# Performance work log

Hardware: AMD Instinct MI355X
Metric: run time of the kernel (lower is better)

Reference implementation:

```python
import jax, jax.numpy as jnp
import numpy as np

# Dims / scalars (from init_kwargs: m = int(T/dt), delta = dt, theta_star = threshold)
M = 50000
N = 500
DELTA = 0.001
GLEAK = 1.0
TAUS = 10.0
THETA_STAR = 1.0
SPIKE_PROB = 0.02  # sparse binary spike raster as produced by time2spike


def setup_inputs() -> dict:
    key = jax.random.key(0)
    k1, k2, k3 = jax.random.split(key, 3)
    # binary spike raster [m, n]
    spikes = (jax.random.uniform(k1, (M, N)) < SPIKE_PROB).astype(jnp.float32)
    # synapse weights ~ N(w_mean=0.01, 0.01)
    w = (0.01 + 0.01 * jax.random.normal(k2, (N,))).astype(jnp.float32)
    # reversal potentials: half excitatory (ex=5), half inhibitory (inh=-1), shuffled
    vrev = jnp.where(jax.random.uniform(k3, (N,)) < 0.5, 5.0, -1.0).astype(jnp.float32)
    return {"spikes": spikes, "w": w, "vrev": vrev}


def reference(spikes, w, vrev):
    dtype = spikes.dtype
    decay = jnp.exp(jnp.asarray(-1.0 / TAUS, dtype))

    # _compute_exp: exp_temp[i] = (exp_temp[i-1] + spikes[i-1]) * exp(-1/taus), exp_temp[0] = 0
    def exp_step(carry, s):
        nxt = (carry + s) * decay
        return nxt, nxt

    _, e_tail = jax.lax.scan(exp_step, jnp.zeros((N,), dtype), spikes[:-1])
    exp_temp = jnp.concatenate([jnp.zeros((1, N), dtype), e_tail], axis=0)  # [M, N]

    # Gsyn_pre = |w| * exp_temp ; Isyn_pre = Vrev * |w| * exp_temp.
    # Only their per-timestep sums over synapses enter the vtr recurrence,
    # so contract over n immediately instead of materializing [M, N] products.
    absw = jnp.abs(w)
    g_sum = exp_temp @ absw            # [M] = sum_j Gsyn_pre[i, j]
    i_sum = exp_temp @ (vrev * absw)   # [M] = sum_j Isyn_pre[i, j]
    a = DELTA * (GLEAK + g_sum)        # per-step leak+conductance factor
    b = DELTA * i_sum                  # per-step input drive

    # _computevtr: if vtr[i-1] < theta: vtr[i] = vtr[i-1]*(1 - a[i-1]) + b[i-1]
    # else vtr[i] stays 0 (state reset after threshold crossing), vtr[0] = 0.
    def vtr_step(v, ab):
        ai, bi = ab
        nxt = jnp.where(v < THETA_STAR, v * (1.0 - ai) + bi, jnp.asarray(0.0, dtype))
        return nxt, nxt

    _, v_tail = jax.lax.scan(vtr_step, jnp.asarray(0.0, dtype), (a[:-1], b[:-1]))
    vtr = jnp.concatenate([jnp.zeros((1,), dtype), v_tail])  # [M]
    return vtr
```

## Files before the change

kernel.cpp:

```cpp
#include <hip/hip_runtime.h>
#include <cmath>

namespace {
constexpr int NELEM  = 50000;
constexpr int NSYN   = 500;
constexpr int NQ4    = 125;
constexpr int T      = 1024;
constexpr int SBLK   = 49;
constexpr int SLOTS  = SBLK * T;
constexpr int CMAXC  = (NELEM - 1) >> 6;
constexpr int NCH_PAD = 784;
constexpr int MAXSEG = 4096;
constexpr int NGRP   = NELEM / 8;
constexpr double DELTA_D = 1.0e-3;
constexpr double THETA_D = 1.0;
constexpr float  DECAY_F = 0.90483741803595957311f;
}

struct WS {
    double2 pq[SLOTS];
    double  eAm[SLOTS], eAg[SLOTS], eAi[SLOTS];
    double  ePl[SLOTS], eQl[SLOTS];
    double  rarr[SLOTS];
    double  gAm[64], gAg[64], gAi[64];
    double  gEm[64], gEg[64], gEi[64];
    double  gPp[64], gPq[64];
    double  gEp[64], gEq[64];
    double  gmaxR[1024];
    double  gbndQ[MAXSEG];
    int     gbnd[MAXSEG];
    int     gnseg;
    int     pad;
    float   swv[SLOTS];
    float   iwv[SLOTS];
};

__global__ __launch_bounds__(256) void k_rowdot(
    const float* __restrict__ spikes,
    const float* __restrict__ w,
    const float* __restrict__ vrev,
    float* __restrict__ swv,
    float* __restrict__ iwv)
{
    const int lane = threadIdx.x & 63;
    const int wv   = threadIdx.x >> 6;
    const int rg   = blockIdx.x * 4 + wv;
    if (rg >= NGRP) return;
    const int row0 = rg * 8;

    const float4* __restrict__ w4 = reinterpret_cast<const float4*>(w);
    const float4* __restrict__ r4 = reinterpret_cast<const float4*>(vrev);
    const int j1 = lane;
    const int j2 = lane + 64;
    const bool has2 = (j2 < NQ4);
    float4 a1 = w4[j1], r1 = r4[j1];
    float4 aw1 = make_float4(fabsf(a1.x), fabsf(a1.y), fabsf(a1.z), fabsf(a1.w));
    float4 ar1 = make_float4(aw1.x * r1.x, aw1.y * r1.y, aw1.z * r1.z, aw1.w * r1.w);
    float4 aw2 = make_float4(0.f, 0.f, 0.f, 0.f), ar2 = aw2;
    if (has2) {
        float4 a2 = w4[j2], r2 = r4[j2];
        aw2 = make_float4(fabsf(a2.x), fabsf(a2.y), fabsf(a2.z), fabsf(a2.w));
        ar2 = make_float4(aw2.x * r2.x, aw2.y * r2.y, aw2.z * r2.z, aw2.w * r2.w);
    }

    float sp[8], ip[8];
#pragma unroll
    for (int r = 0; r < 8; ++r) {
        const float4* __restrict__ srow =
            reinterpret_cast<const float4*>(spikes + (size_t)(row0 + r) * NSYN);
        float4 s1 = srow[j1];
        float a = s1.x * aw1.x + s1.y * aw1.y + s1.z * aw1.z + s1.w * aw1.w;
        float b = s1.x * ar1.x + s1.y * ar1.y + s1.z * ar1.z + s1.w * ar1.w;
        if (has2) {
            float4 s2 = srow[j2];
            a += s2.x * aw2.x + s2.y * aw2.y + s2.z * aw2.z + s2.w * aw2.w;
            b += s2.x * ar2.x + s2.y * ar2.y + s2.z * ar2.z + s2.w * ar2.w;
        }
        sp[r] = a; ip[r] = b;
    }
#pragma unroll
    for (int d = 32; d > 0; d >>= 1) {
#pragma unroll
        for (int r = 0; r < 8; ++r) {
            sp[r] += __shfl_xor(sp[r], d);
            ip[r] += __shfl_xor(ip[r], d);
        }
    }
    if (lane == 0) {
        *reinterpret_cast<float4*>(swv + row0)     = make_float4(sp[0], sp[1], sp[2], sp[3]);
        *reinterpret_cast<float4*>(swv + row0 + 4) = make_float4(sp[4], sp[5], sp[6], sp[7]);
        *reinterpret_cast<float4*>(iwv + row0)     = make_float4(ip[0], ip[1], ip[2], ip[3]);
        *reinterpret_cast<float4*>(iwv + row0 + 4) = make_float4(ip[4], ip[5], ip[6], ip[7]);
    }
}

__global__ __launch_bounds__(1024) void k_scanA(const float* __restrict__ swv,
                                                const float* __restrict__ iwv,
                                                WS* __restrict__ ws)
{
    const int tid = threadIdx.x, lane = tid & 63, wv = tid >> 6, blk = blockIdx.x;
    const int idx = blk * T + tid;
    const bool live = (idx < NELEM);
    const double decay = (double)DECAY_F;
    __shared__ double s_a[16], s_b[16], s_c[16];

    double s = live ? (double)swv[idx] : 0.0;
    double t = live ? (double)iwv[idx] : 0.0;
    double m_in = live ? decay : 1.0;
    double g_in = live ? s * decay : 0.0;
    double i_in = live ? t * decay : 0.0;
#pragma unroll
    for (int d = 1; d < 64; d <<= 1) {
        double pm = __shfl_up(m_in, d);
        double pg = __shfl_up(g_in, d);
        double pi = __shfl_up(i_in, d);
        if (lane >= d) {
            g_in = m_in * pg + g_in;
            i_in = m_in * pi + i_in;
            m_in = pm * m_in;
        }
    }
    if (lane == 63) { s_a[wv] = m_in; s_b[wv] = g_in; s_c[wv] = i_in; }
    __syncthreads();
    if (wv == 0) {
        double wm = (lane < 16) ? s_a[lane] : 1.0;
        double wg = (lane < 16) ? s_b[lane] : 0.0;
        double wi = (lane < 16) ? s_c[lane] : 0.0;
#pragma unroll
        for (int d = 1; d < 16; d <<= 1) {
            double pm = __shfl_up(wm, d);
            double pg = __shfl_up(wg, d);
            double pi = __shfl_up(wi, d);
            if (lane >= d) {
                wg = wm * pg + wg;
                wi = wm * pi + wi;
                wm = pm * wm;
            }
        }
        if (lane < 16) { s_a[lane] = wm; s_b[lane] = wg; s_c[lane] = wi; }
        if (lane == 15) { ws->gAm[blk] = wm; ws->gAg[blk] = wg; ws->gAi[blk] = wi; }
    }
    __syncthreads();
    double em = __shfl_up(m_in, 1), eg = __shfl_up(g_in, 1), ei = __shfl_up(i_in, 1);
    if (lane == 0) { em = 1.0; eg = 0.0; ei = 0.0; }
    if (wv > 0) {
        double qm = s_a[wv - 1], qg = s_b[wv - 1], qi = s_c[wv - 1];
        eg = em * qg + eg;
        ei = em * qi + ei;
        em = qm * em;
    }
    ws->eAm[idx] = em; ws->eAg[idx] = eg; ws->eAi[idx] = ei;
}

__global__ void k_aggA(WS* __restrict__ ws)
{
    const int lane = threadIdx.x;
    double am = (lane < SBLK) ? ws->gAm[lane] : 1.0;
    double ag = (lane < SBLK) ? ws->gAg[lane] : 0.0;
    double ai = (lane < SBLK) ? ws->gAi[lane] : 0.0;
#pragma unroll
    for (int d = 1; d < 64; d <<= 1) {
        double pm = __shfl_up(am, d);
        double pg = __shfl_up(ag, d);
        double pi = __shfl_up(ai, d);
        if (lane >= d) {
            ag = am * pg + ag;
            ai = am * pi + ai;
            am = pm * am;
        }
    }
    double em = __shfl_up(am, 1), eg = __shfl_up(ag, 1), ei = __shfl_up(ai, 1);
    if (lane == 0) { em = 1.0; eg = 0.0; ei = 0.0; }
    if (lane < SBLK) { ws->gEm[lane] = em; ws->gEg[lane] = eg; ws->gEi[lane] = ei; }
}

__global__ __launch_bounds__(1024) void k_scanB(WS* __restrict__ ws)
{
    const int tid = threadIdx.x, lane = tid & 63, wv = tid >> 6, blk = blockIdx.x;
    const int idx = blk * T + tid;
    const bool live = (idx < NELEM);
    __shared__ double s_a[16], s_b[16];

    double em = ws->eAm[idx], eg = ws->eAg[idx], ei = ws->eAi[idx];
    double qm = ws->gEm[blk], qg = ws->gEg[blk], qi = ws->gEi[blk];
    double Eg = em * qg + eg;
    double Ei = em * qi + ei;
    (void)qm;

    double p_in = 1.0, q_in = 0.0;
    if (live) {
        double aa = DELTA_D * (1.0 + Eg);
        double om = 1.0 - aa;
        p_in = om;
        q_in = (DELTA_D * Ei) / om;
    }
#pragma unroll
    for (int d = 1; d < 64; d <<= 1) {
        double pp = __shfl_up(p_in, d);
        double pq = __shfl_up(q_in, d);
        if (lane >= d) {
            q_in = pq + q_in / pp;
            p_in = pp * p_in;
        }
    }
    if (lane == 63) { s_a[wv] = p_in; s_b[wv] = q_in; }
    __syncthreads();
    if (wv == 0) {
        double wp = (lane < 16) ? s_a[lane] : 1.0;
        double wq = (lane < 16) ? s_b[lane] : 0.0;
#pragma unroll
        for (int d = 1; d < 16; d <<= 1) {
            double pp = __shfl_up(wp, d);
            double pq = __shfl_up(wq, d);
            if (lane >= d) {
                wq = pq + wq / pp;
                wp = pp * wp;
            }
        }
        if (lane < 16) { s_a[lane] = wp; s_b[lane] = wq; }
        if (lane == 15) { ws->gPp[blk] = wp; ws->gPq[blk] = wq; }
    }
    __syncthreads();
    double ep = __shfl_up(p_in, 1), eq = __shfl_up(q_in, 1);
    if (lane == 0) { ep = 1.0; eq = 0.0; }
    if (wv > 0) {
        double ap = s_a[wv - 1], aq = s_b[wv - 1];
        eq = aq + eq / ap;
        ep = ap * ep;
    }
    ws->ePl[idx] = ep; ws->eQl[idx] = eq;
}

__global__ void k_aggB(WS* __restrict__ ws)
{
    const int lane = threadIdx.x;
    double ap = (lane < SBLK) ? ws->gPp[lane] : 1.0;
    double aq = (lane < SBLK) ? ws->gPq[lane] : 0.0;
#pragma unroll
    for (int d = 1; d < 64; d <<= 1) {
        double pp = __shfl_up(ap, d);
        double pq = __shfl_up(aq, d);
        if (lane >= d) {
            aq = pq + aq / pp;
            ap = pp * ap;
        }
    }
    double ep = __shfl_up(ap, 1), eq = __shfl_up(aq, 1);
    if (lane == 0) { ep = 1.0; eq = 0.0; }
    if (lane < SBLK) { ws->gEp[lane] = ep; ws->gEq[lane] = eq; }
}

__global__ __launch_bounds__(1024) void k_apply(WS* __restrict__ ws)
{
    const int tid = threadIdx.x, lane = tid & 63, blk = blockIdx.x;
    const int idx = blk * T + tid;
    const bool live = (idx < NELEM);

    double pl = ws->ePl[idx], ql = ws->eQl[idx];
    double ap = ws->gEp[blk], aq = ws->gEq[blk];
    double Q = aq + ql / ap;
    double P = ap * pl;
    ws->pq[idx] = make_double2(P, Q);
    double R = live ? (Q - THETA_D / P) : -1.0e308;
    ws->rarr[idx] = R;
    double mR = R;
#pragma unroll
    for (int d = 32; d > 0; d >>= 1) mR = fmax(mR, __shfl_xor(mR, d));
    if (lane == 0) ws->gmaxR[idx >> 6] = mR;
}

__global__ __launch_bounds__(1024) void k_search(WS* __restrict__ ws)
{
    const int tid = threadIdx.x;
    __shared__ double smax[NCH_PAD];
    __shared__ double s_guard;

    for (int c = tid; c < NCH_PAD; c += T)
        smax[c] = (c <= CMAXC) ? ws->gmaxR[c] : -1.0e308;
    double acc = 0.0;
    for (int i = tid; i < NELEM; i += T) acc += ws->rarr[i];
    for (int i = tid; i < NELEM; i += T) acc += ws->pq[i].y;
    if (acc == -1.2345e300) s_guard = acc;
    __syncthreads();

    if (tid < 64) {
        const int lane = tid;
        int nseg = 1;
        if (lane == 0) { ws->gbnd[0] = 0; ws->gbndQ[0] = 0.0; }
        double Qr = 0.0;
        int pos = 1;
        while (pos < NELEM && nseg < MAXSEG) {
            int c = pos >> 6;
            int i0 = -1;
            while (true) {
                int cf = -1;
                for (int cb = c; cb <= CMAXC; cb += 64) {
                    int cc = cb + lane;
                    bool qy = (cc <= CMAXC) && (smax[cc] >= Qr);
                    unsigned long long m = __ballot(qy);
                    if (m) { cf = cb + __builtin_ctzll(m); break; }
                }
                if (cf < 0) break;
                int i = (cf << 6) + lane;
                bool valid = (i >= pos) && (i < NELEM);
                double rv = valid ? ws->rarr[i] : -1.0e308;
                unsigned long long m2 = __ballot(valid && (rv >= Qr));
                if (m2) { i0 = (cf << 6) + __builtin_ctzll(m2); break; }
                c = cf + 1;
                if (c > CMAXC) break;
            }
            if (i0 < 0) break;
            int nb = i0 + 1;
            if (nb >= NELEM) break;
            Qr = ws->pq[nb].y;
            if (lane == 0) { ws->gbnd[nseg] = nb; ws->gbndQ[nseg] = Qr; }
            nseg++;
            pos = nb + 1;
        }
        if (lane == 0) ws->gnseg = nseg;
    }
}

__global__ __launch_bounds__(1024) void k_fill(const WS* __restrict__ ws,
                                               float* __restrict__ out)
{
    __shared__ int    sb[MAXSEG];
    __shared__ double sq[MAXSEG];
    __shared__ int    s_nseg;
    const int tid = threadIdx.x;
    if (tid == 0) s_nseg = ws->gnseg;
    __syncthreads();
    const int nseg = s_nseg;
    for (int i = tid; i < nseg; i += T) { sb[i] = ws->gbnd[i]; sq[i] = ws->gbndQ[i]; }
    __syncthreads();

    const int idx = blockIdx.x * T + tid;
    if (idx < NELEM) {
        int lo = 0, hi = nseg - 1;
        while (lo < hi) {
            int mid = (lo + hi + 1) >> 1;
            if (sb[mid] <= idx) lo = mid; else hi = mid - 1;
        }
        if (idx == sb[lo]) {
            out[idx] = 0.0f;
        } else {
            double2 pl = ws->pq[idx];
            out[idx] = (float)(pl.x * (pl.y - sq[lo]));
        }
    }
}

extern "C" void kernel_launch(void* const* d_in, const int* in_sizes, int n_in,
                              void* d_out, int out_size, void* d_ws, size_t ws_size,
                              hipStream_t stream) {
    const float* spikes = (const float*)d_in[0];
    const float* w      = (const float*)d_in[1];
    const float* vrev   = (const float*)d_in[2];
    float* out = (float*)d_out;
    WS* ws = (WS*)d_ws;

    hipLaunchKernelGGL(k_rowdot, dim3((NGRP + 3) / 4), dim3(256), 0, stream,
                       spikes, w, vrev, ws->swv, ws->iwv);
    hipLaunchKernelGGL(k_scanA,  dim3(SBLK), dim3(T),  0, stream, ws->swv, ws->iwv, ws);
    hipLaunchKernelGGL(k_aggA,   dim3(1),    dim3(64), 0, stream, ws);
    hipLaunchKernelGGL(k_scanB,  dim3(SBLK), dim3(T),  0, stream, ws);
    hipLaunchKernelGGL(k_aggB,   dim3(1),    dim3(64), 0, stream, ws);
    hipLaunchKernelGGL(k_apply,  dim3(SBLK), dim3(T),  0, stream, ws);
    hipLaunchKernelGGL(k_search, dim3(1),    dim3(T),  0, stream, ws);
    hipLaunchKernelGGL(k_fill,   dim3(SBLK), dim3(T),  0, stream, ws, out);
}
```

Measured before the change: 206.3 us.

## Fuse scan, aggregate and apply stages into one cooperative kernel with grid syncs

Merges the five kernels k_scanA, k_aggA, k_scanB, k_aggB and k_apply into one cooperative kernel that uses grid.sync between phases. Each block rescans the 49 block aggregates itself instead of reading results from a separate kernel. This removes four kernel launches and the intermediate global arrays (eAm/eAg/eAi, ePl/eQl). It also writes Q to a separate contiguous qarr so the search kernel reads it with better access. The cost is two grid-wide barriers, and correctness depends on all 49 blocks being co-resident.

```diff
diff --git a/kernel.cpp b/kernel.cpp
--- a/kernel.cpp
+++ b/kernel.cpp
@@ -1,5 +1,8 @@
 #include <hip/hip_runtime.h>
+#include <hip/hip_cooperative_groups.h>
 #include <cmath>
+
+namespace cg = cooperative_groups;
 
 namespace {
 constexpr int NELEM  = 50000;
@@ -19,13 +22,10 @@
 
 struct WS {
     double2 pq[SLOTS];
-    double  eAm[SLOTS], eAg[SLOTS], eAi[SLOTS];
-    double  ePl[SLOTS], eQl[SLOTS];
     double  rarr[SLOTS];
+    double  qarr[SLOTS];
     double  gAm[64], gAg[64], gAi[64];
-    double  gEm[64], gEg[64], gEi[64];
     double  gPp[64], gPq[64];
-    double  gEp[64], gEq[64];
     double  gmaxR[1024];
     double  gbndQ[MAXSEG];
     int     gbnd[MAXSEG];
@@ -94,15 +94,22 @@
     }
 }
 
-__global__ __launch_bounds__(1024) void k_scanA(const float* __restrict__ swv,
-                                                const float* __restrict__ iwv,
-                                                WS* __restrict__ ws)
+__global__ __launch_bounds__(1024) void k_scanfused(
+    const float* __restrict__ swv,
+    const float* __restrict__ iwv,
+    WS* __restrict__ ws)
 {
-    const int tid = threadIdx.x, lane = tid & 63, wv = tid >> 6, blk = blockIdx.x;
-    const int idx = blk * T + tid;
+    cg::grid_group grid = cg::this_grid();
+    const int tid  = threadIdx.x;
+    const int lane = tid & 63;
+    const int wv   = tid >> 6;
+    const int blk  = blockIdx.x;
+    const int idx  = blk * T + tid;
     const bool live = (idx < NELEM);
     const double decay = (double)DECAY_F;
+
     __shared__ double s_a[16], s_b[16], s_c[16];
+    __shared__ double s_e[6];
 
     double s = live ? (double)swv[idx] : 0.0;
     double t = live ? (double)iwv[idx] : 0.0;
@@ -140,52 +147,50 @@
         if (lane < 16) { s_a[lane] = wm; s_b[lane] = wg; s_c[lane] = wi; }
         if (lane == 15) { ws->gAm[blk] = wm; ws->gAg[blk] = wg; ws->gAi[blk] = wi; }
     }
-    __syncthreads();
-    double em = __shfl_up(m_in, 1), eg = __shfl_up(g_in, 1), ei = __shfl_up(i_in, 1);
-    if (lane == 0) { em = 1.0; eg = 0.0; ei = 0.0; }
-    if (wv > 0) {
-        double qm = s_a[wv - 1], qg = s_b[wv - 1], qi = s_c[wv - 1];
-        eg = em * qg + eg;
-        ei = em * qi + ei;
-        em = qm * em;
-    }
-    ws->eAm[idx] = em; ws->eAg[idx] = eg; ws->eAi[idx] = ei;
-}
-
-__global__ void k_aggA(WS* __restrict__ ws)
-{
-    const int lane = threadIdx.x;
-    double am = (lane < SBLK) ? ws->gAm[lane] : 1.0;
-    double ag = (lane < SBLK) ? ws->gAg[lane] : 0.0;
-    double ai = (lane < SBLK) ? ws->gAi[lane] : 0.0;
-#pragma unroll
-    for (int d = 1; d < 64; d <<= 1) {
-        double pm = __shfl_up(am, d);
-        double pg = __shfl_up(ag, d);
-        double pi = __shfl_up(ai, d);
-        if (lane >= d) {
-            ag = am * pg + ag;
-            ai = am * pi + ai;
-            am = pm * am;
-        }
-    }
-    double em = __shfl_up(am, 1), eg = __shfl_up(ag, 1), ei = __shfl_up(ai, 1);
-    if (lane == 0) { em = 1.0; eg = 0.0; ei = 0.0; }
-    if (lane < SBLK) { ws->gEm[lane] = em; ws->gEg[lane] = eg; ws->gEi[lane] = ei; }
-}
-
-__global__ __launch_bounds__(1024) void k_scanB(WS* __restrict__ ws)
-{
-    const int tid = threadIdx.x, lane = tid & 63, wv = tid >> 6, blk = blockIdx.x;
-    const int idx = blk * T + tid;
-    const bool live = (idx < NELEM);
-    __shared__ double s_a[16], s_b[16];
-
-    double em = ws->eAm[idx], eg = ws->eAg[idx], ei = ws->eAi[idx];
-    double qm = ws->gEm[blk], qg = ws->gEg[blk], qi = ws->gEi[blk];
-    double Eg = em * qg + eg;
-    double Ei = em * qi + ei;
-    (void)qm;
+    __threadfence();
+    grid.sync();
+
+    if (wv == 0) {
+        double am = (lane < SBLK) ? ws->gAm[lane] : 1.0;
+        double ag = (lane < SBLK) ? ws->gAg[lane] : 0.0;
+        double ai = (lane < SBLK) ? ws->gAi[lane] : 0.0;
+#pragma unroll
+        for (int d = 1; d < 64; d <<= 1) {
+            double pm = __shfl_up(am, d);
+            double pg = __shfl_up(ag, d);
+            double pi = __shfl_up(ai, d);
+            if (lane >= d) {
+                ag = am * pg + ag;
+                ai = am * pi + ai;
+                am = pm * am;
+            }
+        }
+        if (blk == 0) {
+            if (lane == 0) { s_e[0] = 1.0; s_e[1] = 0.0; s_e[2] = 0.0; }
+        } else if (lane == blk - 1) {
+            s_e[0] = am; s_e[1] = ag; s_e[2] = ai;
+        }
+    }
+    __syncthreads();
+
+    double Eg, Ei;
+    {
+        double em = __shfl_up(m_in, 1), eg = __shfl_up(g_in, 1), ei = __shfl_up(i_in, 1);
+        if (lane == 0) { em = 1.0; eg = 0.0; ei = 0.0; }
+        if (wv > 0) {
+            double qm = s_a[wv - 1], qg = s_b[wv - 1], qi = s_c[wv - 1];
+            eg = em * qg + eg;
+            ei = em * qi + ei;
+            em = qm * em;
+        }
+        {
+            double qg = s_e[1], qi = s_e[2];
+            eg = em * qg + eg;
+            ei = em * qi + ei;
+        }
+        Eg = eg; Ei = ei;
+    }
+    __syncthreads();
 
     double p_in = 1.0, q_in = 0.0;
     if (live) {
@@ -220,7 +225,29 @@
         if (lane < 16) { s_a[lane] = wp; s_b[lane] = wq; }
         if (lane == 15) { ws->gPp[blk] = wp; ws->gPq[blk] = wq; }
     }
-    __syncthreads();
+    __threadfence();
+    grid.sync();
+
+    if (wv == 0) {
+        double ap = (lane < SBLK) ? ws->gPp[lane] : 1.0;
+        double aq = (lane < SBLK) ? ws->gPq[lane] : 0.0;
+#pragma unroll
+        for (int d = 1; d < 64; d <<= 1) {
+            double pp = __shfl_up(ap, d);
+            double pq = __shfl_up(aq, d);
+            if (lane >= d) {
+                aq = pq + aq / pp;
+                ap = pp * ap;
+            }
+        }
+        if (blk == 0) {
+            if (lane == 0) { s_e[3] = 1.0; s_e[4] = 0.0; }
+        } else if (lane == blk - 1) {
+            s_e[3] = ap; s_e[4] = aq;
+        }
+    }
+    __syncthreads();
+
     double ep = __shfl_up(p_in, 1), eq = __shfl_up(q_in, 1);
     if (lane == 0) { ep = 1.0; eq = 0.0; }
     if (wv > 0) {
@@ -228,39 +255,12 @@
         eq = aq + eq / ap;
         ep = ap * ep;
     }
-    ws->ePl[idx] = ep; ws->eQl[idx] = eq;
-}
-
-__global__ void k_aggB(WS* __restrict__ ws)
-{
-    const int lane = threadIdx.x;
-    double ap = (lane < SBLK) ? ws->gPp[lane] : 1.0;
-    double aq = (lane < SBLK) ? ws->gPq[lane] : 0.0;
-#pragma unroll
-    for (int d = 1; d < 64; d <<= 1) {
-        double pp = __shfl_up(ap, d);
-        double pq = __shfl_up(aq, d);
-        if (lane >= d) {
-            aq = pq + aq / pp;
-            ap = pp * ap;
-        }
-    }
-    double ep = __shfl_up(ap, 1), eq = __shfl_up(aq, 1);
-    if (lane == 0) { ep = 1.0; eq = 0.0; }
-    if (lane < SBLK) { ws->gEp[lane] = ep; ws->gEq[lane] = eq; }
-}
-
-__global__ __launch_bounds__(1024) void k_apply(WS* __restrict__ ws)
-{
-    const int tid = threadIdx.x, lane = tid & 63, blk = blockIdx.x;
-    const int idx = blk * T + tid;
-    const bool live = (idx < NELEM);
-
-    double pl = ws->ePl[idx], ql = ws->eQl[idx];
-    double ap = ws->gEp[blk], aq = ws->gEq[blk];
-    double Q = aq + ql / ap;
-    double P = ap * pl;
-    ws->pq[idx] = make_double2(P, Q);
+    double ap = s_e[3], aq = s_e[4];
+    double Q = aq + eq / ap;
+    double P = ap * ep;
+
+    ws->pq[idx]   = make_double2(P, Q);
+    ws->qarr[idx] = Q;
     double R = live ? (Q - THETA_D / P) : -1.0e308;
     ws->rarr[idx] = R;
     double mR = R;
@@ -273,14 +273,13 @@
 {
     const int tid = threadIdx.x;
     __shared__ double smax[NCH_PAD];
-    __shared__ double s_guard;
 
     for (int c = tid; c < NCH_PAD; c += T)
         smax[c] = (c <= CMAXC) ? ws->gmaxR[c] : -1.0e308;
     double acc = 0.0;
     for (int i = tid; i < NELEM; i += T) acc += ws->rarr[i];
-    for (int i = tid; i < NELEM; i += T) acc += ws->pq[i].y;
-    if (acc == -1.2345e300) s_guard = acc;
+    for (int i = tid; i < NELEM; i += T) acc += ws->qarr[i];
+    if (acc == -1.2345e300) ws->pad = 1;
     __syncthreads();
 
     if (tid < 64) {
@@ -312,7 +311,7 @@
             if (i0 < 0) break;
             int nb = i0 + 1;
             if (nb >= NELEM) break;
-            Qr = ws->pq[nb].y;
+            Qr = ws->qarr[nb];
             if (lane == 0) { ws->gbnd[nseg] = nb; ws->gbndQ[nseg] = Qr; }
             nseg++;
             pos = nb + 1;
@@ -361,11 +360,13 @@
 
     hipLaunchKernelGGL(k_rowdot, dim3((NGRP + 3) / 4), dim3(256), 0, stream,
                        spikes, w, vrev, ws->swv, ws->iwv);
-    hipLaunchKernelGGL(k_scanA,  dim3(SBLK), dim3(T),  0, stream, ws->swv, ws->iwv, ws);
-    hipLaunchKernelGGL(k_aggA,   dim3(1),    dim3(64), 0, stream, ws);
-    hipLaunchKernelGGL(k_scanB,  dim3(SBLK), dim3(T),  0, stream, ws);
-    hipLaunchKernelGGL(k_aggB,   dim3(1),    dim3(64), 0, stream, ws);
-    hipLaunchKernelGGL(k_apply,  dim3(SBLK), dim3(T),  0, stream, ws);
-    hipLaunchKernelGGL(k_search, dim3(1),    dim3(T),  0, stream, ws);
-    hipLaunchKernelGGL(k_fill,   dim3(SBLK), dim3(T),  0, stream, ws, out);
-}
+
+    const float* swv_p = ws->swv;
+    const float* iwv_p = ws->iwv;
+    void* args[] = { (void*)&swv_p, (void*)&iwv_p, (void*)&ws };
+    hipLaunchCooperativeKernel((const void*)k_scanfused, dim3(SBLK), dim3(T),
+                               args, 0, stream);
+
+    hipLaunchKernelGGL(k_search, dim3(1),    dim3(T), 0, stream, ws);
+    hipLaunchKernelGGL(k_fill,   dim3(SBLK), dim3(T), 0, stream, ws, out);
+}
```

Result: slower. 269.7 us (+30.7%).

## Fold block-aggregate scans into consumer kernels and split Q into its own array

Applied to the files above, without the earlier changes.

Removes the two single-wave aggregation kernels by having every block of scanB and apply redundantly scan the per-block aggregates in shared memory and pick its own exclusive prefix. This cuts two kernel launches and their serialisation gaps from the chain. It also adds a contiguous Q array so the serial search reads dense doubles instead of strided double2 elements, and batches the spike-row loads in rowdot ahead of the arithmetic for more memory-level parallelism. The cost is some redundant small scans per block and an extra array write.

```diff
diff --git a/kernel.cpp b/kernel.cpp
--- a/kernel.cpp
+++ b/kernel.cpp
@@ -19,13 +19,12 @@
 
 struct WS {
     double2 pq[SLOTS];
+    double  rarr[SLOTS];
+    double  qarr[SLOTS];
     double  eAm[SLOTS], eAg[SLOTS], eAi[SLOTS];
     double  ePl[SLOTS], eQl[SLOTS];
-    double  rarr[SLOTS];
     double  gAm[64], gAg[64], gAi[64];
-    double  gEm[64], gEg[64], gEi[64];
     double  gPp[64], gPq[64];
-    double  gEp[64], gEq[64];
     double  gmaxR[1024];
     double  gbndQ[MAXSEG];
     int     gbnd[MAXSEG];
@@ -63,18 +62,22 @@
         ar2 = make_float4(aw2.x * r2.x, aw2.y * r2.y, aw2.z * r2.z, aw2.w * r2.w);
     }
 
-    float sp[8], ip[8];
+    float4 s1[8], s2[8];
 #pragma unroll
     for (int r = 0; r < 8; ++r) {
         const float4* __restrict__ srow =
             reinterpret_cast<const float4*>(spikes + (size_t)(row0 + r) * NSYN);
-        float4 s1 = srow[j1];
-        float a = s1.x * aw1.x + s1.y * aw1.y + s1.z * aw1.z + s1.w * aw1.w;
-        float b = s1.x * ar1.x + s1.y * ar1.y + s1.z * ar1.z + s1.w * ar1.w;
+        s1[r] = srow[j1];
+        if (has2) s2[r] = srow[j2];
+    }
+    float sp[8], ip[8];
+#pragma unroll
+    for (int r = 0; r < 8; ++r) {
+        float a = s1[r].x * aw1.x + s1[r].y * aw1.y + s1[r].z * aw1.z + s1[r].w * aw1.w;
+        float b = s1[r].x * ar1.x + s1[r].y * ar1.y + s1[r].z * ar1.z + s1[r].w * ar1.w;
         if (has2) {
-            float4 s2 = srow[j2];
-            a += s2.x * aw2.x + s2.y * aw2.y + s2.z * aw2.z + s2.w * aw2.w;
-            b += s2.x * ar2.x + s2.y * ar2.y + s2.z * ar2.z + s2.w * ar2.w;
+            a += s2[r].x * aw2.x + s2[r].y * aw2.y + s2[r].z * aw2.z + s2[r].w * aw2.w;
+            b += s2[r].x * ar2.x + s2[r].y * ar2.y + s2[r].z * ar2.z + s2[r].w * ar2.w;
         }
         sp[r] = a; ip[r] = b;
     }
@@ -94,9 +97,7 @@
     }
 }
 
-__global__ __launch_bounds__(1024) void k_scanA(const float* __restrict__ swv,
-                                                const float* __restrict__ iwv,
-                                                WS* __restrict__ ws)
+__global__ __launch_bounds__(1024) void k_scanA(WS* __restrict__ ws)
 {
     const int tid = threadIdx.x, lane = tid & 63, wv = tid >> 6, blk = blockIdx.x;
     const int idx = blk * T + tid;
@@ -104,8 +105,8 @@
     const double decay = (double)DECAY_F;
     __shared__ double s_a[16], s_b[16], s_c[16];
 
-    double s = live ? (double)swv[idx] : 0.0;
-    double t = live ? (double)iwv[idx] : 0.0;
+    double s = live ? (double)ws->swv[idx] : 0.0;
+    double t = live ? (double)ws->iwv[idx] : 0.0;
     double m_in = live ? decay : 1.0;
     double g_in = live ? s * decay : 0.0;
     double i_in = live ? t * decay : 0.0;
@@ -152,40 +153,40 @@
     ws->eAm[idx] = em; ws->eAg[idx] = eg; ws->eAi[idx] = ei;
 }
 
-__global__ void k_aggA(WS* __restrict__ ws)
-{
-    const int lane = threadIdx.x;
-    double am = (lane < SBLK) ? ws->gAm[lane] : 1.0;
-    double ag = (lane < SBLK) ? ws->gAg[lane] : 0.0;
-    double ai = (lane < SBLK) ? ws->gAi[lane] : 0.0;
-#pragma unroll
-    for (int d = 1; d < 64; d <<= 1) {
-        double pm = __shfl_up(am, d);
-        double pg = __shfl_up(ag, d);
-        double pi = __shfl_up(ai, d);
-        if (lane >= d) {
-            ag = am * pg + ag;
-            ai = am * pi + ai;
-            am = pm * am;
-        }
-    }
-    double em = __shfl_up(am, 1), eg = __shfl_up(ag, 1), ei = __shfl_up(ai, 1);
-    if (lane == 0) { em = 1.0; eg = 0.0; ei = 0.0; }
-    if (lane < SBLK) { ws->gEm[lane] = em; ws->gEg[lane] = eg; ws->gEi[lane] = ei; }
-}
-
 __global__ __launch_bounds__(1024) void k_scanB(WS* __restrict__ ws)
 {
     const int tid = threadIdx.x, lane = tid & 63, wv = tid >> 6, blk = blockIdx.x;
     const int idx = blk * T + tid;
     const bool live = (idx < NELEM);
     __shared__ double s_a[16], s_b[16];
+    __shared__ double s_e[2];
+
+    if (wv == 0) {
+        double am = (lane < SBLK) ? ws->gAm[lane] : 1.0;
+        double ag = (lane < SBLK) ? ws->gAg[lane] : 0.0;
+        double ai = (lane < SBLK) ? ws->gAi[lane] : 0.0;
+#pragma unroll
+        for (int d = 1; d < 64; d <<= 1) {
+            double pm = __shfl_up(am, d);
+            double pg = __shfl_up(ag, d);
+            double pi = __shfl_up(ai, d);
+            if (lane >= d) {
+                ag = am * pg + ag;
+                ai = am * pi + ai;
+                am = pm * am;
+            }
+        }
+        if (blk == 0) {
+            if (lane == 0) { s_e[0] = 0.0; s_e[1] = 0.0; }
+        } else if (lane == blk - 1) {
+            s_e[0] = ag; s_e[1] = ai;
+        }
+    }
+    __syncthreads();
 
     double em = ws->eAm[idx], eg = ws->eAg[idx], ei = ws->eAi[idx];
-    double qm = ws->gEm[blk], qg = ws->gEg[blk], qi = ws->gEi[blk];
-    double Eg = em * qg + eg;
-    double Ei = em * qi + ei;
-    (void)qm;
+    double Eg = em * s_e[0] + eg;
+    double Ei = em * s_e[1] + ei;
 
     double p_in = 1.0, q_in = 0.0;
     if (live) {
@@ -231,36 +232,39 @@
     ws->ePl[idx] = ep; ws->eQl[idx] = eq;
 }
 
-__global__ void k_aggB(WS* __restrict__ ws)
-{
-    const int lane = threadIdx.x;
-    double ap = (lane < SBLK) ? ws->gPp[lane] : 1.0;
-    double aq = (lane < SBLK) ? ws->gPq[lane] : 0.0;
-#pragma unroll
-    for (int d = 1; d < 64; d <<= 1) {
-        double pp = __shfl_up(ap, d);
-        double pq = __shfl_up(aq, d);
-        if (lane >= d) {
-            aq = pq + aq / pp;
-            ap = pp * ap;
-        }
-    }
-    double ep = __shfl_up(ap, 1), eq = __shfl_up(aq, 1);
-    if (lane == 0) { ep = 1.0; eq = 0.0; }
-    if (lane < SBLK) { ws->gEp[lane] = ep; ws->gEq[lane] = eq; }
-}
-
 __global__ __launch_bounds__(1024) void k_apply(WS* __restrict__ ws)
 {
     const int tid = threadIdx.x, lane = tid & 63, blk = blockIdx.x;
     const int idx = blk * T + tid;
     const bool live = (idx < NELEM);
+    __shared__ double s_e[2];
+
+    if (tid < 64) {
+        double ap = (lane < SBLK) ? ws->gPp[lane] : 1.0;
+        double aq = (lane < SBLK) ? ws->gPq[lane] : 0.0;
+#pragma unroll
+        for (int d = 1; d < 64; d <<= 1) {
+            double pp = __shfl_up(ap, d);
+            double pq = __shfl_up(aq, d);
+            if (lane >= d) {
+                aq = pq + aq / pp;
+                ap = pp * ap;
+            }
+        }
+        if (blk == 0) {
+            if (lane == 0) { s_e[0] = 1.0; s_e[1] = 0.0; }
+        } else if (lane == blk - 1) {
+            s_e[0] = ap; s_e[1] = aq;
+        }
+    }
+    __syncthreads();
 
     double pl = ws->ePl[idx], ql = ws->eQl[idx];
-    double ap = ws->gEp[blk], aq = ws->gEq[blk];
+    double ap = s_e[0], aq = s_e[1];
     double Q = aq + ql / ap;
     double P = ap * pl;
-    ws->pq[idx] = make_double2(P, Q);
+    ws->pq[idx]   = make_double2(P, Q);
+    ws->qarr[idx] = Q;
     double R = live ? (Q - THETA_D / P) : -1.0e308;
     ws->rarr[idx] = R;
     double mR = R;
@@ -273,14 +277,13 @@
 {
     const int tid = threadIdx.x;
     __shared__ double smax[NCH_PAD];
-    __shared__ double s_guard;
 
     for (int c = tid; c < NCH_PAD; c += T)
         smax[c] = (c <= CMAXC) ? ws->gmaxR[c] : -1.0e308;
     double acc = 0.0;
     for (int i = tid; i < NELEM; i += T) acc += ws->rarr[i];
-    for (int i = tid; i < NELEM; i += T) acc += ws->pq[i].y;
-    if (acc == -1.2345e300) s_guard = acc;
+    for (int i = tid; i < NELEM; i += T) acc += ws->qarr[i];
+    if (acc == -1.2345e300) ws->pad = 1;
     __syncthreads();
 
     if (tid < 64) {
@@ -312,7 +315,7 @@
             if (i0 < 0) break;
             int nb = i0 + 1;
             if (nb >= NELEM) break;
-            Qr = ws->pq[nb].y;
+            Qr = ws->qarr[nb];
             if (lane == 0) { ws->gbnd[nseg] = nb; ws->gbndQ[nseg] = Qr; }
             nseg++;
             pos = nb + 1;
@@ -361,11 +364,9 @@
 
     hipLaunchKernelGGL(k_rowdot, dim3((NGRP + 3) / 4), dim3(256), 0, stream,
                        spikes, w, vrev, ws->swv, ws->iwv);
-    hipLaunchKernelGGL(k_scanA,  dim3(SBLK), dim3(T),  0, stream, ws->swv, ws->iwv, ws);
-    hipLaunchKernelGGL(k_aggA,   dim3(1),    dim3(64), 0, stream, ws);
-    hipLaunchKernelGGL(k_scanB,  dim3(SBLK), dim3(T),  0, stream, ws);
-    hipLaunchKernelGGL(k_aggB,   dim3(1),    dim3(64), 0, stream, ws);
-    hipLaunchKernelGGL(k_apply,  dim3(SBLK), dim3(T),  0, stream, ws);
-    hipLaunchKernelGGL(k_search, dim3(1),    dim3(T),  0, stream, ws);
-    hipLaunchKernelGGL(k_fill,   dim3(SBLK), dim3(T),  0, stream, ws, out);
-}
+    hipLaunchKernelGGL(k_scanA,  dim3(SBLK), dim3(T), 0, stream, ws);
+    hipLaunchKernelGGL(k_scanB,  dim3(SBLK), dim3(T), 0, stream, ws);
+    hipLaunchKernelGGL(k_apply,  dim3(SBLK), dim3(T), 0, stream, ws);
+    hipLaunchKernelGGL(k_search, dim3(1),    dim3(T), 0, stream, ws);
+    hipLaunchKernelGGL(k_fill,   dim3(SBLK), dim3(T), 0, stream, ws, out);
+}
```

Result: slower. 215.4 us (+4.4%).
